# Optimization experiments

Measured on AMD Instinct MI355X. Metric: run time of the kernel, lower is better.

The kernel has to match this reference:

```python
import math
import jax, jax.numpy as jnp
import numpy as np

B, N, D, L = 8, 4096, 512, 64


def setup_inputs() -> dict:
    key = jax.random.key(0)
    ks = jax.random.split(key, 8)
    feats = jax.random.normal(ks[0], (B, N, D), dtype=jnp.float32)
    coords = jax.random.uniform(ks[1], (B, N, 2), dtype=jnp.float32)
    mask = jax.random.bernoulli(ks[2], 0.5, (B, N))  # True = padding (excluded)
    z = jax.random.normal(ks[3], (L, D), dtype=jnp.float32) * 0.02
    # xavier_uniform with gain=0.05 for square DxD weights: bound = gain*sqrt(6/(2D))
    bound = 0.05 * math.sqrt(6.0 / (2 * D))
    Wq = jax.random.uniform(ks[4], (D, D), minval=-bound, maxval=bound, dtype=jnp.float32)
    Wk = jax.random.uniform(ks[5], (D, D), minval=-bound, maxval=bound, dtype=jnp.float32)
    Wv = jax.random.uniform(ks[6], (D, D), minval=-bound, maxval=bound, dtype=jnp.float32)
    Wo = jax.random.uniform(ks[7], (D, D), minval=-bound, maxval=bound, dtype=jnp.float32)
    bo = jnp.zeros((D,), dtype=jnp.float32)
    return {"feats": feats, "coords": coords, "mask": mask, "z": z,
            "Wq": Wq, "Wk": Wk, "Wv": Wv, "Wo": Wo, "bo": bo}


def reference(feats, coords, mask, z, Wq, Wk, Wv, Wo, bo):
    Bb, Nn, Dd = feats.shape
    Ll = z.shape[0]
    temp = math.sqrt(Dd)
    q_all = z @ Wq.T  # [L, D] — one query per learned token

    def per_sample(f, m):
        nvalid = jnp.sum(~m)
        # stable sort: valid tokens (mask=False) first, original order preserved
        order = jnp.argsort(m.astype(jnp.int32), stable=True)
        sf = f[order]  # [N, D], first nvalid rows are the valid feats
        mu = sf.mean(-1, keepdims=True)
        var = sf.var(-1, keepdims=True)
        ln = (sf - mu) / jnp.sqrt(var + 1e-5)
        # segment assignment: seg_size = max(1, nvalid // L); token i -> segment i//seg_size
        seg_size = jnp.maximum(1, nvalid // Ll)
        pos = jnp.arange(Nn)
        seg = pos // seg_size
        tok_valid = (pos < nvalid) & (seg < Ll)  # tokens past L*seg_size are dropped (matches torch)
        seg_id = jnp.where(tok_valid, seg, Ll)  # dummy segment L for excluded tokens
        K = ln @ Wk.T  # [N, D]
        V = ln @ Wv.T  # [N, D]
        logits = jnp.clip(jnp.sum(q_all[jnp.minimum(seg, Ll - 1)] * K, -1) / temp, -5.0, 5.0)
        m_seg = jax.ops.segment_max(jnp.where(tok_valid, logits, -jnp.inf), seg_id, num_segments=Ll + 1)
        m_safe = jnp.where(jnp.isfinite(m_seg), m_seg, 0.0)
        e = jnp.where(tok_valid, jnp.exp(logits - m_safe[seg_id]), 0.0)
        denom = jax.ops.segment_sum(e, seg_id, num_segments=Ll + 1)[:Ll]            # [L]
        num = jax.ops.segment_sum(e[:, None] * V, seg_id, num_segments=Ll + 1)[:Ll]  # [L, D]
        nonempty = denom > 0
        Zattn = jnp.where(nonempty[:, None], num / jnp.maximum(denom, 1e-30)[:, None], z)
        out = Zattn @ Wo.T + bo
        return jnp.where(nvalid == 0, z, out)

    return jax.vmap(per_sample)(feats, mask)
```

## Files before the change

kernel.cpp:

```cpp
#include <hip/hip_runtime.h>
#include <math.h>

#define Bn 8
#define Nn 4096
#define Dn 512
#define Ln 64

template<int TN, bool BT, int NPART, bool SCALE>
__device__ __forceinline__ void gemm_tile(
    const float* __restrict__ A, size_t apstride, int m0,
    const float* __restrict__ B, int n0, int kbase, int ksteps,
    const float* __restrict__ sv,
    float* __restrict__ dst,
    float (*As)[68], float (*Bs)[132], int tid)
{
    const int ty = tid >> 4;
    const int tx = tid & 15;
    float acc[4][TN / 16];
    #pragma unroll
    for (int m = 0; m < 4; m++)
        #pragma unroll
        for (int n = 0; n < TN / 16; n++) acc[m][n] = 0.f;

    for (int s = 0; s < ksteps; s++) {
        const int k0 = kbase + s * 16;
        {
            int r = tid >> 2, kq = tid & 3;
            float4 v = *(const float4*)&A[(size_t)(m0 + r) * Dn + k0 + kq * 4];
            #pragma unroll
            for (int p = 1; p < NPART; p++) {
                float4 w = *(const float4*)&A[(size_t)p * apstride +
                                              (size_t)(m0 + r) * Dn + k0 + kq * 4];
                v.x += w.x; v.y += w.y; v.z += w.z; v.w += w.w;
            }
            if (SCALE) { float sc = sv[r]; v.x *= sc; v.y *= sc; v.z *= sc; v.w *= sc; }
            As[kq * 4 + 0][r] = v.x;
            As[kq * 4 + 1][r] = v.y;
            As[kq * 4 + 2][r] = v.z;
            As[kq * 4 + 3][r] = v.w;
        }
        #pragma unroll
        for (int rep = 0; rep < TN / 64; rep++) {
            int lin = tid + rep * 256;
            if (!BT) {
                int kk = lin / (TN / 4), jq = lin % (TN / 4);
                *(float4*)&Bs[kk][jq * 4] =
                    *(const float4*)&B[(size_t)(k0 + kk) * Dn + n0 + jq * 4];
            } else {
                int j = lin >> 2, kq = lin & 3;
                float4 v = *(const float4*)&B[(size_t)(n0 + j) * Dn + k0 + kq * 4];
                Bs[kq * 4 + 0][j] = v.x;
                Bs[kq * 4 + 1][j] = v.y;
                Bs[kq * 4 + 2][j] = v.z;
                Bs[kq * 4 + 3][j] = v.w;
            }
        }
        __syncthreads();
        #pragma unroll
        for (int kk = 0; kk < 16; kk++) {
            float4 a = *(const float4*)&As[kk][ty * 4];
            float av[4] = {a.x, a.y, a.z, a.w};
            if (TN == 64) {
                float4 b = *(const float4*)&Bs[kk][tx * 4];
                float bv[4] = {b.x, b.y, b.z, b.w};
                #pragma unroll
                for (int m = 0; m < 4; m++)
                    #pragma unroll
                    for (int n = 0; n < 4; n++) acc[m][n] += av[m] * bv[n];
            } else {
                float4 b0 = *(const float4*)&Bs[kk][tx * 8];
                float4 b1 = *(const float4*)&Bs[kk][tx * 8 + 4];
                float bv[8] = {b0.x, b0.y, b0.z, b0.w, b1.x, b1.y, b1.z, b1.w};
                #pragma unroll
                for (int m = 0; m < 4; m++)
                    #pragma unroll
                    for (int n = 0; n < 8; n++) acc[m][n % (TN/16)] += av[m] * bv[n];
            }
        }
        __syncthreads();
    }
    #pragma unroll
    for (int m = 0; m < 4; m++) {
        size_t base = (size_t)(m0 + ty * 4 + m) * Dn + n0;
        if (TN == 64) {
            float4 o = {acc[m][0], acc[m][1], acc[m][2], acc[m][3]};
            *(float4*)&dst[base + tx * 4] = o;
        } else {
            float4 o0 = {acc[m][0], acc[m][1], acc[m][2], acc[m][3]};
            float4 o1 = {acc[m][4], acc[m][5], acc[m][6], acc[m][7]};
            *(float4*)&dst[base + tx * 8] = o0;
            *(float4*)&dst[base + tx * 8 + 4] = o1;
        }
    }
}

__global__ void __launch_bounds__(256) kA_prep(
    const float* __restrict__ Wo, const float* __restrict__ Wv,
    const float* __restrict__ z,  const float* __restrict__ Wq,
    const unsigned char* __restrict__ maskbytes,
    float* __restrict__ wp, float* __restrict__ qp, float* __restrict__ wozp,
    int* __restrict__ nvalid, int* __restrict__ idx)
{
    __shared__ float As[16][68];
    __shared__ float Bs[16][132];
    __shared__ int scanbuf[256];
    __shared__ int cflags[4];

    int tid = threadIdx.x;
    int gb = blockIdx.x;

    if (gb < 256) {
        int ks = gb & 7;  int t = gb >> 3;
        int rt = t >> 2, ct = t & 3;
        gemm_tile<128, false, 1, false>(Wo, 0, rt * 64, Wv, ct * 128,
                                        ks * 64, 4, nullptr,
                                        wp + (size_t)ks * 262144, As, Bs, tid);
        return;
    }
    if (gb < 288) {
        int t = gb - 256; int ks = t & 3; int nt = t >> 2;
        gemm_tile<64, true, 1, false>(z, 0, 0, Wq, nt * 64,
                                      ks * 128, 8, nullptr,
                                      qp + (size_t)ks * 32768, As, Bs, tid);
        return;
    }
    if (gb < 320) {
        int t = gb - 288; int ks = t & 3; int nt = t >> 2;
        gemm_tile<64, true, 1, false>(z, 0, 0, Wo, nt * 64,
                                      ks * 128, 8, nullptr,
                                      wozp + (size_t)ks * 32768, As, Bs, tid);
        return;
    }

    int b = gb - 320;
    if (tid == 0) { cflags[0] = 0; cflags[1] = 0; cflags[2] = 0; }
    __syncthreads();
    int lge2 = 0, lb1 = 0, lm = 0;
    for (int p = tid; p < 4096; p += 256) {
        unsigned int v = maskbytes[p];
        if (v > 1u) lge2 = 1;
        if (v != 0u) {
            if ((p & 3) == 1) lb1 = 1;
            if ((p & 3) != 0) lm = 1;
        }
    }
    if (lge2) atomicOr(&cflags[0], 1);
    if (lb1)  atomicOr(&cflags[1], 1);
    if (lm)   atomicOr(&cflags[2], 1);
    __syncthreads();
    if (tid == 0) cflags[3] = cflags[0] ? (cflags[1] ? 2 : 4) : (cflags[2] ? 1 : 4);
    __syncthreads();
    int w = cflags[3];

    int base = tid * 16;
    int cnt = 0;
    int validbits[16];
    for (int e = 0; e < 16; e++) {
        int i = base + e;
        size_t byteoff = ((size_t)b * Nn + i) * (size_t)w;
        unsigned int nz = 0;
        for (int q = 0; q < w; q++) nz |= maskbytes[byteoff + q];
        int valid = (nz == 0) ? 1 : 0;
        validbits[e] = valid;
        cnt += valid;
    }
    scanbuf[tid] = cnt;
    __syncthreads();
    for (int off = 1; off < 256; off <<= 1) {
        int v = (tid >= off) ? scanbuf[tid - off] : 0;
        __syncthreads();
        scanbuf[tid] += v;
        __syncthreads();
    }
    int pos = scanbuf[tid] - cnt;
    for (int e = 0; e < 16; e++) {
        if (validbits[e]) { idx[b * Nn + pos] = base + e; pos++; }
    }
    if (tid == 255) nvalid[b] = scanbuf[255];
}

__global__ void __launch_bounds__(256) kB_qk(
    const float* __restrict__ qp, const float* __restrict__ Wk,
    const float* __restrict__ wp,
    float* __restrict__ qkp, float* __restrict__ wov)
{
    __shared__ float As[16][68];
    __shared__ float Bs[16][132];
    int tid = threadIdx.x;
    int gb = blockIdx.x;
    if (gb < 64) {
        int ks = gb & 7; int nt = gb >> 3;
        gemm_tile<64, false, 4, false>(qp, 32768, 0, Wk, nt * 64,
                                       ks * 64, 4, nullptr,
                                       qkp + (size_t)ks * 32768, As, Bs, tid);
        return;
    }
    int lin = (gb - 64) * 256 + tid;
    float4 v = {0.f, 0.f, 0.f, 0.f};
    #pragma unroll
    for (int p = 0; p < 8; p++) {
        float4 w = *(const float4*)&wp[(size_t)p * 262144 + (size_t)lin * 4];
        v.x += w.x; v.y += w.y; v.z += w.z; v.w += w.w;
    }
    *(float4*)&wov[(size_t)lin * 4] = v;
}

__global__ void __launch_bounds__(256) kE_tokens(
    const float* __restrict__ feats, const int* __restrict__ idx,
    const int* __restrict__ nvalid, const float* __restrict__ qkp,
    float* __restrict__ s_out, float* __restrict__ den_out)
{
    __shared__ float sred[4 * Dn];
    __shared__ float dred[4];
    int tid = threadIdx.x;
    int wv = tid >> 6;
    int lane = tid & 63;
    int b = blockIdx.x / Ln;
    int l = blockIdx.x % Ln;
    int nv = nvalid[b];
    int seg_size = nv / Ln; if (seg_size < 1) seg_size = 1;
    int used = Ln * seg_size; if (used > nv) used = nv;
    int r0 = l * seg_size;
    int r1 = r0 + seg_size; if (r1 > used) r1 = used;

    float4 qa = {0.f,0.f,0.f,0.f}, qb = {0.f,0.f,0.f,0.f};
    #pragma unroll
    for (int p = 0; p < 8; p++) {
        const float4* q4 = (const float4*)(qkp + (size_t)p * 32768 +
                                           (size_t)l * Dn + lane * 8);
        float4 a = q4[0], c = q4[1];
        qa.x += a.x; qa.y += a.y; qa.z += a.z; qa.w += a.w;
        qb.x += c.x; qb.y += c.y; qb.z += c.z; qb.w += c.w;
    }
    float qf[8] = {qa.x, qa.y, qa.z, qa.w, qb.x, qb.y, qb.z, qb.w};

    float sacc[8] = {0,0,0,0,0,0,0,0};
    float dacc = 0.f;
    const float inv_d = 1.0f / (float)Dn;
    const float inv_temp = 1.0f / 22.62741699796952f;

    for (int r = r0 + wv * 2; r < r1; r += 8) {
        int has2 = (r + 1 < r1);
        int t0 = idx[b * Nn + r];
        int t1 = has2 ? idx[b * Nn + r + 1] : t0;
        const float4* p0 = (const float4*)(feats + ((size_t)b * Nn + t0) * Dn + lane * 8);
        const float4* p1 = (const float4*)(feats + ((size_t)b * Nn + t1) * Dn + lane * 8);
        float4 xa0 = p0[0], xb0 = p0[1];
        float4 xa1 = p1[0], xb1 = p1[1];
        float x0[8] = {xa0.x, xa0.y, xa0.z, xa0.w, xb0.x, xb0.y, xb0.z, xb0.w};
        float x1[8] = {xa1.x, xa1.y, xa1.z, xa1.w, xb1.x, xb1.y, xb1.z, xb1.w};
        float sum0 = 0.f, ssq0 = 0.f, sum1 = 0.f, ssq1 = 0.f;
        #pragma unroll
        for (int j = 0; j < 8; j++) {
            sum0 += x0[j]; ssq0 += x0[j] * x0[j];
            sum1 += x1[j]; ssq1 += x1[j] * x1[j];
        }
        #pragma unroll
        for (int off = 32; off > 0; off >>= 1) {
            sum0 += __shfl_xor(sum0, off);
            ssq0 += __shfl_xor(ssq0, off);
            sum1 += __shfl_xor(sum1, off);
            ssq1 += __shfl_xor(ssq1, off);
        }
        float mu0 = sum0 * inv_d, mu1 = sum1 * inv_d;
        float rstd0 = rsqrtf(ssq0 * inv_d - mu0 * mu0 + 1e-5f);
        float rstd1 = rsqrtf(ssq1 * inv_d - mu1 * mu1 + 1e-5f);
        float ln0[8], ln1[8];
        float dot0 = 0.f, dot1 = 0.f;
        #pragma unroll
        for (int j = 0; j < 8; j++) {
            ln0[j] = (x0[j] - mu0) * rstd0; dot0 += ln0[j] * qf[j];
            ln1[j] = (x1[j] - mu1) * rstd1; dot1 += ln1[j] * qf[j];
        }
        #pragma unroll
        for (int off = 32; off > 0; off >>= 1) {
            dot0 += __shfl_xor(dot0, off);
            dot1 += __shfl_xor(dot1, off);
        }
        float lg0 = fminf(5.0f, fmaxf(-5.0f, dot0 * inv_temp));
        float lg1 = fminf(5.0f, fmaxf(-5.0f, dot1 * inv_temp));
        float e0 = expf(lg0);
        float e1 = has2 ? expf(lg1) : 0.f;
        #pragma unroll
        for (int j = 0; j < 8; j++) sacc[j] += e0 * ln0[j] + e1 * ln1[j];
        dacc += e0 + e1;
    }

    #pragma unroll
    for (int j = 0; j < 8; j++) sred[wv * Dn + lane * 8 + j] = sacc[j];
    if (lane == 0) dred[wv] = dacc;
    __syncthreads();
    for (int e = tid; e < Dn; e += 256) {
        float v = sred[e] + sred[Dn + e] + sred[2 * Dn + e] + sred[3 * Dn + e];
        s_out[(size_t)blockIdx.x * Dn + e] = v;
    }
    if (tid == 0) den_out[blockIdx.x] = dred[0] + dred[1] + dred[2] + dred[3];
}

__global__ void __launch_bounds__(256) kG_gemm(
    const float* __restrict__ s, const float* __restrict__ den,
    const float* __restrict__ wov, float* __restrict__ op)
{
    __shared__ float As[16][68];
    __shared__ float Bs[16][132];
    __shared__ float ssv[64];
    int tid = threadIdx.x;
    int gb = blockIdx.x;
    int ks = gb & 7; int t = gb >> 3;
    int rt = t >> 2, ct = t & 3;
    int m0 = rt * 64;
    if (tid < 64) {
        float dv = den[m0 + tid];
        ssv[tid] = (dv > 0.f) ? 1.f / dv : 0.f;
    }
    __syncthreads();
    gemm_tile<128, true, 1, true>(s, 0, m0, wov, ct * 128,
                                  ks * 64, 4, ssv,
                                  op + (size_t)ks * 262144, As, Bs, tid);
}

__global__ void __launch_bounds__(256) kH_epilogue(
    const float* __restrict__ op, const float* __restrict__ den,
    const int* __restrict__ nvalid, const float* __restrict__ wozp,
    const float* __restrict__ z, const float* __restrict__ bo,
    float* __restrict__ out)
{
    int lin = blockIdx.x * 256 + threadIdx.x;
    int row = lin >> 7;
    int col = (lin & 127) * 4;
    int b = row >> 6, l = row & 63;
    float4 v;
    if (nvalid[b] == 0) {
        v = *(const float4*)&z[(size_t)l * Dn + col];
    } else {
        float4 bv = *(const float4*)&bo[col];
        float dv = den[row];
        if (dv > 0.f) {
            float4 a = {0.f, 0.f, 0.f, 0.f};
            #pragma unroll
            for (int p = 0; p < 8; p++) {
                float4 w = *(const float4*)&op[(size_t)p * 262144 + (size_t)row * Dn + col];
                a.x += w.x; a.y += w.y; a.z += w.z; a.w += w.w;
            }
            v.x = a.x + bv.x; v.y = a.y + bv.y; v.z = a.z + bv.z; v.w = a.w + bv.w;
        } else {
            float4 a = {0.f, 0.f, 0.f, 0.f};
            #pragma unroll
            for (int p = 0; p < 4; p++) {
                float4 w = *(const float4*)&wozp[(size_t)p * 32768 + (size_t)l * Dn + col];
                a.x += w.x; a.y += w.y; a.z += w.z; a.w += w.w;
            }
            v.x = a.x + bv.x; v.y = a.y + bv.y; v.z = a.z + bv.z; v.w = a.w + bv.w;
        }
    }
    *(float4*)&out[(size_t)row * Dn + col] = v;
}

extern "C" void kernel_launch(void* const* d_in, const int* in_sizes, int n_in,
                              void* d_out, int out_size, void* d_ws, size_t ws_size,
                              hipStream_t stream) {
    const float* feats = (const float*)d_in[0];
    const unsigned char* maskb = (const unsigned char*)d_in[2];
    const float* z  = (const float*)d_in[3];
    const float* Wq = (const float*)d_in[4];
    const float* Wk = (const float*)d_in[5];
    const float* Wv = (const float*)d_in[6];
    const float* Wo = (const float*)d_in[7];
    const float* bo = (const float*)d_in[8];
    float* out = (float*)d_out;

    int*   nvalid = (int*)d_ws;
    int*   idx    = nvalid + 64;
    float* fbase  = (float*)(idx + Bn * Nn);
    float* qp     = fbase;
    float* wozp   = qp   + 4 * 32768;
    float* qkp    = wozp + 4 * 32768;
    float* wov    = qkp  + 8 * 32768;
    float* sbuf   = wov  + 262144;
    float* den    = sbuf + 262144;
    float* wp     = den  + 1024;
    float* op     = wp;

    kA_prep<<<328, 256, 0, stream>>>(Wo, Wv, z, Wq, maskb, wp, qp, wozp, nvalid, idx);
    kB_qk<<<320, 256, 0, stream>>>(qp, Wk, wp, qkp, wov);
    kE_tokens<<<Bn * Ln, 256, 0, stream>>>(feats, idx, nvalid, qkp, sbuf, den);
    kG_gemm<<<256, 256, 0, stream>>>(sbuf, den, wov, op);
    kH_epilogue<<<256, 256, 0, stream>>>(op, den, nvalid, wozp, z, bo, out);
}
```

Before: 147.4 us.

## Fuse output GEMM with epilogue and shrink wov reduction grid

```diff
diff --git a/kernel.cpp b/kernel.cpp
--- a/kernel.cpp
+++ b/kernel.cpp
@@ -195,14 +195,18 @@
                                        qkp + (size_t)ks * 32768, As, Bs, tid);
         return;
     }
-    int lin = (gb - 64) * 256 + tid;
-    float4 v = {0.f, 0.f, 0.f, 0.f};
-    #pragma unroll
-    for (int p = 0; p < 8; p++) {
-        float4 w = *(const float4*)&wp[(size_t)p * 262144 + (size_t)lin * 4];
-        v.x += w.x; v.y += w.y; v.z += w.z; v.w += w.w;
-    }
-    *(float4*)&wov[(size_t)lin * 4] = v;
+    int base4 = (gb - 64) * 1024;
+    #pragma unroll
+    for (int i = 0; i < 4; i++) {
+        int lin = base4 + i * 256 + tid;
+        float4 v = {0.f, 0.f, 0.f, 0.f};
+        #pragma unroll
+        for (int p = 0; p < 8; p++) {
+            float4 w = *(const float4*)&wp[(size_t)p * 262144 + (size_t)lin * 4];
+            v.x += w.x; v.y += w.y; v.z += w.z; v.w += w.w;
+        }
+        *(float4*)&wov[(size_t)lin * 4] = v;
+    }
 }
 
 __global__ void __launch_bounds__(256) kE_tokens(
@@ -297,63 +301,86 @@
     if (tid == 0) den_out[blockIdx.x] = dred[0] + dred[1] + dred[2] + dred[3];
 }
 
-__global__ void __launch_bounds__(256) kG_gemm(
+__global__ void __launch_bounds__(256) kF_final(
     const float* __restrict__ s, const float* __restrict__ den,
-    const float* __restrict__ wov, float* __restrict__ op)
+    const int* __restrict__ nvalid, const float* __restrict__ wov,
+    const float* __restrict__ wozp, const float* __restrict__ z,
+    const float* __restrict__ bo, float* __restrict__ out)
 {
-    __shared__ float As[16][68];
-    __shared__ float Bs[16][132];
-    __shared__ float ssv[64];
+    __shared__ float As[16][34];
+    __shared__ float Bs[16][34];
+    __shared__ float sinv[32];
+    __shared__ float sden[32];
     int tid = threadIdx.x;
-    int gb = blockIdx.x;
-    int ks = gb & 7; int t = gb >> 3;
-    int rt = t >> 2, ct = t & 3;
-    int m0 = rt * 64;
-    if (tid < 64) {
+    int bi = blockIdx.x >> 4;
+    int bj = blockIdx.x & 15;
+    int m0 = bi * 32, n0 = bj * 32;
+    if (tid < 32) {
         float dv = den[m0 + tid];
-        ssv[tid] = (dv > 0.f) ? 1.f / dv : 0.f;
-    }
-    __syncthreads();
-    gemm_tile<128, true, 1, true>(s, 0, m0, wov, ct * 128,
-                                  ks * 64, 4, ssv,
-                                  op + (size_t)ks * 262144, As, Bs, tid);
-}
-
-__global__ void __launch_bounds__(256) kH_epilogue(
-    const float* __restrict__ op, const float* __restrict__ den,
-    const int* __restrict__ nvalid, const float* __restrict__ wozp,
-    const float* __restrict__ z, const float* __restrict__ bo,
-    float* __restrict__ out)
-{
-    int lin = blockIdx.x * 256 + threadIdx.x;
-    int row = lin >> 7;
-    int col = (lin & 127) * 4;
-    int b = row >> 6, l = row & 63;
-    float4 v;
-    if (nvalid[b] == 0) {
-        v = *(const float4*)&z[(size_t)l * Dn + col];
-    } else {
-        float4 bv = *(const float4*)&bo[col];
-        float dv = den[row];
-        if (dv > 0.f) {
-            float4 a = {0.f, 0.f, 0.f, 0.f};
-            #pragma unroll
-            for (int p = 0; p < 8; p++) {
-                float4 w = *(const float4*)&op[(size_t)p * 262144 + (size_t)row * Dn + col];
-                a.x += w.x; a.y += w.y; a.z += w.z; a.w += w.w;
-            }
-            v.x = a.x + bv.x; v.y = a.y + bv.y; v.z = a.z + bv.z; v.w = a.w + bv.w;
+        sden[tid] = dv;
+        sinv[tid] = (dv > 0.f) ? 1.f / dv : 0.f;
+    }
+    __syncthreads();
+
+    int ty = tid >> 4;
+    int tx = tid & 15;
+    float a00 = 0.f, a01 = 0.f, a10 = 0.f, a11 = 0.f;
+
+    for (int k0 = 0; k0 < Dn; k0 += 16) {
+        if (tid < 128) {
+            int r = tid >> 2, kq = tid & 3;
+            float4 v = *(const float4*)&s[(size_t)(m0 + r) * Dn + k0 + kq * 4];
+            float sc = sinv[r];
+            As[kq * 4 + 0][r] = v.x * sc;
+            As[kq * 4 + 1][r] = v.y * sc;
+            As[kq * 4 + 2][r] = v.z * sc;
+            As[kq * 4 + 3][r] = v.w * sc;
         } else {
-            float4 a = {0.f, 0.f, 0.f, 0.f};
+            int t2 = tid - 128;
+            int j = t2 >> 2, kq = t2 & 3;
+            float4 v = *(const float4*)&wov[(size_t)(n0 + j) * Dn + k0 + kq * 4];
+            Bs[kq * 4 + 0][j] = v.x;
+            Bs[kq * 4 + 1][j] = v.y;
+            Bs[kq * 4 + 2][j] = v.z;
+            Bs[kq * 4 + 3][j] = v.w;
+        }
+        __syncthreads();
+        #pragma unroll
+        for (int kk = 0; kk < 16; kk++) {
+            float2 a = *(const float2*)&As[kk][ty * 2];
+            float2 b = *(const float2*)&Bs[kk][tx * 2];
+            a00 += a.x * b.x; a01 += a.x * b.y;
+            a10 += a.y * b.x; a11 += a.y * b.y;
+        }
+        __syncthreads();
+    }
+
+    float accs[2][2] = {{a00, a01}, {a10, a11}};
+    int col0 = n0 + tx * 2;
+    float2 bv = *(const float2*)&bo[col0];
+    #pragma unroll
+    for (int mm = 0; mm < 2; mm++) {
+        int rl = ty * 2 + mm;
+        int row = m0 + rl;
+        int b = row >> 6, l = row & 63;
+        float2 o;
+        if (nvalid[b] == 0) {
+            o = *(const float2*)&z[(size_t)l * Dn + col0];
+        } else if (sden[rl] > 0.f) {
+            o.x = accs[mm][0] + bv.x;
+            o.y = accs[mm][1] + bv.y;
+        } else {
+            float wx = 0.f, wy = 0.f;
             #pragma unroll
             for (int p = 0; p < 4; p++) {
-                float4 w = *(const float4*)&wozp[(size_t)p * 32768 + (size_t)l * Dn + col];
-                a.x += w.x; a.y += w.y; a.z += w.z; a.w += w.w;
+                float2 w = *(const float2*)&wozp[(size_t)p * 32768 + (size_t)l * Dn + col0];
+                wx += w.x; wy += w.y;
             }
-            v.x = a.x + bv.x; v.y = a.y + bv.y; v.z = a.z + bv.z; v.w = a.w + bv.w;
-        }
-    }
-    *(float4*)&out[(size_t)row * Dn + col] = v;
+            o.x = wx + bv.x;
+            o.y = wy + bv.y;
+        }
+        *(float2*)&out[(size_t)row * Dn + col0] = o;
+    }
 }
 
 extern "C" void kernel_launch(void* const* d_in, const int* in_sizes, int n_in,
@@ -379,11 +406,9 @@
     float* sbuf   = wov  + 262144;
     float* den    = sbuf + 262144;
     float* wp     = den  + 1024;
-    float* op     = wp;
 
     kA_prep<<<328, 256, 0, stream>>>(Wo, Wv, z, Wq, maskb, wp, qp, wozp, nvalid, idx);
-    kB_qk<<<320, 256, 0, stream>>>(qp, Wk, wp, qkp, wov);
+    kB_qk<<<128, 256, 0, stream>>>(qp, Wk, wp, qkp, wov);
     kE_tokens<<<Bn * Ln, 256, 0, stream>>>(feats, idx, nvalid, qkp, sbuf, den);
-    kG_gemm<<<256, 256, 0, stream>>>(sbuf, den, wov, op);
-    kH_epilogue<<<256, 256, 0, stream>>>(op, den, nvalid, wozp, z, bo, out);
-}
+    kF_final<<<256, 256, 0, stream>>>(sbuf, den, nvalid, wov, wozp, z, bo, out);
+}
```

New measurement: 152.6 us. +3.6%, slower.

## Drop precomputed Wo·Wv product; apply Wv then Wo as two small GEMMs

Applied to the files above, without the earlier changes.

```diff
diff --git a/kernel.cpp b/kernel.cpp
--- a/kernel.cpp
+++ b/kernel.cpp
@@ -95,10 +95,10 @@
 }
 
 __global__ void __launch_bounds__(256) kA_prep(
-    const float* __restrict__ Wo, const float* __restrict__ Wv,
-    const float* __restrict__ z,  const float* __restrict__ Wq,
+    const float* __restrict__ z, const float* __restrict__ Wq,
+    const float* __restrict__ Wo,
     const unsigned char* __restrict__ maskbytes,
-    float* __restrict__ wp, float* __restrict__ qp, float* __restrict__ wozp,
+    float* __restrict__ qp, float* __restrict__ wozp,
     int* __restrict__ nvalid, int* __restrict__ idx)
 {
     __shared__ float As[16][68];
@@ -109,30 +109,22 @@
     int tid = threadIdx.x;
     int gb = blockIdx.x;
 
-    if (gb < 256) {
-        int ks = gb & 7;  int t = gb >> 3;
-        int rt = t >> 2, ct = t & 3;
-        gemm_tile<128, false, 1, false>(Wo, 0, rt * 64, Wv, ct * 128,
-                                        ks * 64, 4, nullptr,
-                                        wp + (size_t)ks * 262144, As, Bs, tid);
-        return;
-    }
-    if (gb < 288) {
-        int t = gb - 256; int ks = t & 3; int nt = t >> 2;
+    if (gb < 32) {
+        int ks = gb & 3; int nt = gb >> 2;
         gemm_tile<64, true, 1, false>(z, 0, 0, Wq, nt * 64,
                                       ks * 128, 8, nullptr,
                                       qp + (size_t)ks * 32768, As, Bs, tid);
         return;
     }
-    if (gb < 320) {
-        int t = gb - 288; int ks = t & 3; int nt = t >> 2;
+    if (gb < 64) {
+        int t = gb - 32; int ks = t & 3; int nt = t >> 2;
         gemm_tile<64, true, 1, false>(z, 0, 0, Wo, nt * 64,
                                       ks * 128, 8, nullptr,
                                       wozp + (size_t)ks * 32768, As, Bs, tid);
         return;
     }
 
-    int b = gb - 320;
+    int b = gb - 64;
     if (tid == 0) { cflags[0] = 0; cflags[1] = 0; cflags[2] = 0; }
     __syncthreads();
     int lge2 = 0, lb1 = 0, lm = 0;
@@ -181,28 +173,16 @@
 
 __global__ void __launch_bounds__(256) kB_qk(
     const float* __restrict__ qp, const float* __restrict__ Wk,
-    const float* __restrict__ wp,
-    float* __restrict__ qkp, float* __restrict__ wov)
+    float* __restrict__ qkp)
 {
     __shared__ float As[16][68];
     __shared__ float Bs[16][132];
     int tid = threadIdx.x;
     int gb = blockIdx.x;
-    if (gb < 64) {
-        int ks = gb & 7; int nt = gb >> 3;
-        gemm_tile<64, false, 4, false>(qp, 32768, 0, Wk, nt * 64,
-                                       ks * 64, 4, nullptr,
-                                       qkp + (size_t)ks * 32768, As, Bs, tid);
-        return;
-    }
-    int lin = (gb - 64) * 256 + tid;
-    float4 v = {0.f, 0.f, 0.f, 0.f};
-    #pragma unroll
-    for (int p = 0; p < 8; p++) {
-        float4 w = *(const float4*)&wp[(size_t)p * 262144 + (size_t)lin * 4];
-        v.x += w.x; v.y += w.y; v.z += w.z; v.w += w.w;
-    }
-    *(float4*)&wov[(size_t)lin * 4] = v;
+    int ks = gb & 7; int nt = gb >> 3;
+    gemm_tile<64, false, 4, false>(qp, 32768, 0, Wk, nt * 64,
+                                   ks * 64, 4, nullptr,
+                                   qkp + (size_t)ks * 32768, As, Bs, tid);
 }
 
 __global__ void __launch_bounds__(256) kE_tokens(
@@ -297,63 +277,112 @@
     if (tid == 0) den_out[blockIdx.x] = dred[0] + dred[1] + dred[2] + dred[3];
 }
 
-__global__ void __launch_bounds__(256) kG_gemm(
+__global__ void __launch_bounds__(256) kT_gemm(
     const float* __restrict__ s, const float* __restrict__ den,
-    const float* __restrict__ wov, float* __restrict__ op)
+    const float* __restrict__ Wv, float* __restrict__ tp)
 {
     __shared__ float As[16][68];
     __shared__ float Bs[16][132];
     __shared__ float ssv[64];
     int tid = threadIdx.x;
     int gb = blockIdx.x;
-    int ks = gb & 7; int t = gb >> 3;
-    int rt = t >> 2, ct = t & 3;
+    int ks = gb & 1; int t = gb >> 1;
+    int rt = t >> 3, ct = t & 7;
     int m0 = rt * 64;
     if (tid < 64) {
         float dv = den[m0 + tid];
         ssv[tid] = (dv > 0.f) ? 1.f / dv : 0.f;
     }
     __syncthreads();
-    gemm_tile<128, true, 1, true>(s, 0, m0, wov, ct * 128,
-                                  ks * 64, 4, ssv,
-                                  op + (size_t)ks * 262144, As, Bs, tid);
-}
-
-__global__ void __launch_bounds__(256) kH_epilogue(
-    const float* __restrict__ op, const float* __restrict__ den,
+    gemm_tile<64, true, 1, true>(s, 0, m0, Wv, ct * 64,
+                                 ks * 256, 16, ssv,
+                                 tp + (size_t)ks * 262144, As, Bs, tid);
+}
+
+__global__ void __launch_bounds__(256) kF_final(
+    const float* __restrict__ tp, const float* __restrict__ den,
     const int* __restrict__ nvalid, const float* __restrict__ wozp,
-    const float* __restrict__ z, const float* __restrict__ bo,
-    float* __restrict__ out)
-{
-    int lin = blockIdx.x * 256 + threadIdx.x;
-    int row = lin >> 7;
-    int col = (lin & 127) * 4;
-    int b = row >> 6, l = row & 63;
-    float4 v;
-    if (nvalid[b] == 0) {
-        v = *(const float4*)&z[(size_t)l * Dn + col];
-    } else {
-        float4 bv = *(const float4*)&bo[col];
-        float dv = den[row];
-        if (dv > 0.f) {
-            float4 a = {0.f, 0.f, 0.f, 0.f};
+    const float* __restrict__ z, const float* __restrict__ Wo,
+    const float* __restrict__ bo, float* __restrict__ out)
+{
+    __shared__ float As[16][68];
+    __shared__ float Bs[16][68];
+    __shared__ float sden[64];
+    int tid = threadIdx.x;
+    int rt = blockIdx.x >> 3;
+    int ct = blockIdx.x & 7;
+    int m0 = rt * 64, n0 = ct * 64;
+    if (tid < 64) sden[tid] = den[m0 + tid];
+    __syncthreads();
+
+    int ty = tid >> 4;
+    int tx = tid & 15;
+    float acc[4][4];
+    #pragma unroll
+    for (int m = 0; m < 4; m++)
+        #pragma unroll
+        for (int n = 0; n < 4; n++) acc[m][n] = 0.f;
+
+    for (int s = 0; s < 32; s++) {
+        int k0 = s * 16;
+        {
+            int r = tid >> 2, kq = tid & 3;
+            float4 v = *(const float4*)&tp[(size_t)(m0 + r) * Dn + k0 + kq * 4];
+            float4 w = *(const float4*)&tp[262144 + (size_t)(m0 + r) * Dn + k0 + kq * 4];
+            v.x += w.x; v.y += w.y; v.z += w.z; v.w += w.w;
+            As[kq * 4 + 0][r] = v.x;
+            As[kq * 4 + 1][r] = v.y;
+            As[kq * 4 + 2][r] = v.z;
+            As[kq * 4 + 3][r] = v.w;
+        }
+        {
+            int j = tid >> 2, kq = tid & 3;
+            float4 v = *(const float4*)&Wo[(size_t)(n0 + j) * Dn + k0 + kq * 4];
+            Bs[kq * 4 + 0][j] = v.x;
+            Bs[kq * 4 + 1][j] = v.y;
+            Bs[kq * 4 + 2][j] = v.z;
+            Bs[kq * 4 + 3][j] = v.w;
+        }
+        __syncthreads();
+        #pragma unroll
+        for (int kk = 0; kk < 16; kk++) {
+            float4 a = *(const float4*)&As[kk][ty * 4];
+            float4 b = *(const float4*)&Bs[kk][tx * 4];
+            float av[4] = {a.x, a.y, a.z, a.w};
+            float bv[4] = {b.x, b.y, b.z, b.w};
             #pragma unroll
-            for (int p = 0; p < 8; p++) {
-                float4 w = *(const float4*)&op[(size_t)p * 262144 + (size_t)row * Dn + col];
-                a.x += w.x; a.y += w.y; a.z += w.z; a.w += w.w;
-            }
-            v.x = a.x + bv.x; v.y = a.y + bv.y; v.z = a.z + bv.z; v.w = a.w + bv.w;
+            for (int m = 0; m < 4; m++)
+                #pragma unroll
+                for (int n = 0; n < 4; n++) acc[m][n] += av[m] * bv[n];
+        }
+        __syncthreads();
+    }
+
+    int nvb = nvalid[rt];
+    int col0 = n0 + tx * 4;
+    float4 bv4 = *(const float4*)&bo[col0];
+    #pragma unroll
+    for (int m = 0; m < 4; m++) {
+        int rl = ty * 4 + m;
+        int row = m0 + rl;
+        float4 o;
+        if (nvb == 0) {
+            o = *(const float4*)&z[(size_t)rl * Dn + col0];
+        } else if (sden[rl] > 0.f) {
+            o.x = acc[m][0] + bv4.x; o.y = acc[m][1] + bv4.y;
+            o.z = acc[m][2] + bv4.z; o.w = acc[m][3] + bv4.w;
         } else {
             float4 a = {0.f, 0.f, 0.f, 0.f};
             #pragma unroll
             for (int p = 0; p < 4; p++) {
-                float4 w = *(const float4*)&wozp[(size_t)p * 32768 + (size_t)l * Dn + col];
+                float4 w = *(const float4*)&wozp[(size_t)p * 32768 + (size_t)rl * Dn + col0];
                 a.x += w.x; a.y += w.y; a.z += w.z; a.w += w.w;
             }
-            v.x = a.x + bv.x; v.y = a.y + bv.y; v.z = a.z + bv.z; v.w = a.w + bv.w;
-        }
-    }
-    *(float4*)&out[(size_t)row * Dn + col] = v;
+            o.x = a.x + bv4.x; o.y = a.y + bv4.y;
+            o.z = a.z + bv4.z; o.w = a.w + bv4.w;
+        }
+        *(float4*)&out[(size_t)row * Dn + col0] = o;
+    }
 }
 
 extern "C" void kernel_launch(void* const* d_in, const int* in_sizes, int n_in,
@@ -375,15 +404,13 @@
     float* qp     = fbase;
     float* wozp   = qp   + 4 * 32768;
     float* qkp    = wozp + 4 * 32768;
-    float* wov    = qkp  + 8 * 32768;
-    float* sbuf   = wov  + 262144;
+    float* sbuf   = qkp  + 8 * 32768;
     float* den    = sbuf + 262144;
-    float* wp     = den  + 1024;
-    float* op     = wp;
-
-    kA_prep<<<328, 256, 0, stream>>>(Wo, Wv, z, Wq, maskb, wp, qp, wozp, nvalid, idx);
-    kB_qk<<<320, 256, 0, stream>>>(qp, Wk, wp, qkp, wov);
+    float* tp     = den  + 1024;
+
+    kA_prep<<<72, 256, 0, stream>>>(z, Wq, Wo, maskb, qp, wozp, nvalid, idx);
+    kB_qk<<<64, 256, 0, stream>>>(qp, Wk, qkp);
     kE_tokens<<<Bn * Ln, 256, 0, stream>>>(feats, idx, nvalid, qkp, sbuf, den);
-    kG_gemm<<<256, 256, 0, stream>>>(sbuf, den, wov, op);
-    kH_epilogue<<<256, 256, 0, stream>>>(op, den, nvalid, wozp, z, bo, out);
-}
+    kT_gemm<<<128, 256, 0, stream>>>(sbuf, den, Wv, tp);
+    kF_final<<<64, 256, 0, stream>>>(tp, den, nvalid, wozp, z, Wo, bo, out);
+}
```

After: 171.8 us. +16.6%, slower.
